# Kernel tuning notes

Hardware: AMD Instinct MI355X
Metric: run time of the kernel (lower is better)

Reference implementation:

```python
import jax, jax.numpy as jnp
import numpy as np

CR = 32  # channels // reduction

def setup_inputs() -> dict:
    key = jax.random.key(0)
    k1, k2 = jax.random.split(key)
    x = jax.random.normal(k1, (1, 64, 8, 32, 32), dtype=jnp.float32)
    W = jax.random.normal(k2, (CR, 64), dtype=jnp.float32) * (1.0 / np.sqrt(64.0))
    bias = jnp.zeros((CR,), dtype=jnp.float32)
    return {"x": x, "W": W, "bias": bias}

def reference(x, W, bias):
    b, c, d, h, w = x.shape
    cr = W.shape[0]
    n = d * h * w
    # 1x1x1 Conv3d == per-voxel linear projection over channels
    x_red = jnp.einsum('oc,bcdhw->bodhw', W, x) + bias[None, :, None, None, None]
    q = x_red.reshape(b, cr, n)          # [b, cr, N]
    k = q                                 # shared projection (q == k)
    v = x.reshape(b, c, n)               # [b, c, N]
    # attn[b, i, j] = <q[:, i], k[:, j]>, softmax over j (dim=2)
    attn = jnp.einsum('bci,bcj->bij', q, k) / jnp.sqrt(jnp.float32(cr))
    attn = jax.nn.softmax(attn, axis=2)
    # out[b, c, m] = sum_n v[b, c, n] * attn[b, n, m]  (torch.bmm(v, attn))
    out = jnp.einsum('bcn,bnm->bcm', v, attn)
    out = out.reshape(b, c, d, h, w)
    return out + x
```

## Files before the change

kernel.cpp:

```cpp
#include <hip/hip_runtime.h>

#define N_TOK 8192

typedef _Float16 f16x8 __attribute__((ext_vector_type(8)));
typedef _Float16 f16x4 __attribute__((ext_vector_type(4)));
typedef float    f32x4 __attribute__((ext_vector_type(4)));

__device__ __forceinline__ f32x4 mfma_k32(f16x8 a, f16x8 b, f32x4 c) {
  return __builtin_amdgcn_mfma_f32_16x16x32_f16(a, b, c, 0, 0, 0);
}
__device__ __forceinline__ f32x4 mfma_k16(f16x4 a, f16x4 b, f32x4 c) {
  return __builtin_amdgcn_mfma_f32_16x16x16f16(a, b, c, 0, 0, 0);
}

#define QSCALE 0.50500977f

__global__ __launch_bounds__(1024) void prep_kernel(
    const float* __restrict__ x, const float* __restrict__ W,
    const float* __restrict__ bias, _Float16* __restrict__ qe,
    _Float16* __restrict__ vht, float* __restrict__ Ln,
    float* __restrict__ out) {
  __shared__ float Wl[32 * 65];
  __shared__ float xl[64 * 36];
  int t = threadIdx.x, b = blockIdx.x;
  int n0 = b * 32;
  if (b < 8) Ln[b * 1024 + t] = 0.f;
  for (int i = t; i < 2048; i += 1024) Wl[(i >> 6) * 65 + (i & 63)] = W[i];
  if (t < 512) {
    int c = t >> 3, j4 = t & 7;
    f32x4 v = *(const f32x4*)(x + c * N_TOK + n0 + j4 * 4);
    *(f32x4*)&xl[c * 36 + j4 * 4] = v;
    *(f32x4*)(out + c * N_TOK + n0 + j4 * 4) = v;
    f16x4 hv;
#pragma unroll
    for (int j = 0; j < 4; ++j) hv[j] = (_Float16)v[j];
    int q = j4 & 3, h = j4 >> 2;
    *(f16x4*)(vht + b * 2048 + c * 32 + q * 8 + h * 4) = hv;
  }
  __syncthreads();
  int nl = t >> 5, o = t & 31;
  float a0 = bias[o], a1 = 0.f;
#pragma unroll
  for (int c = 0; c < 32; ++c) {
    a0 = fmaf(Wl[o * 65 + c], xl[c * 36 + nl], a0);
    a1 = fmaf(Wl[o * 65 + 32 + c], xl[(32 + c) * 36 + nl], a1);
  }
  qe[(n0 + nl) * 32 + o] = (_Float16)((a0 + a1) * QSCALE);
}

__global__ __launch_bounds__(1024) void pass1_kernel(
    const _Float16* __restrict__ qe, float* __restrict__ Ln) {
  __shared__ float Lp[16][64];
  int t = threadIdx.x, b = blockIdx.x;
  int w = t >> 6, lane = t & 63, quad = lane >> 4, l15 = lane & 15;
  int n0 = (b >> 1) * 64;
  int mbase = (b & 1) * 4096 + w * 256;
  f16x8 af[4];
#pragma unroll
  for (int g = 0; g < 4; ++g)
    af[g] = *(const f16x8*)(qe + (n0 + g * 16 + l15) * 32 + quad * 8);
  f32x4 sums[4];
#pragma unroll
  for (int g = 0; g < 4; ++g) sums[g] = f32x4{0.f, 0.f, 0.f, 0.f};
  for (int mt = 0; mt < 8; ++mt) {
    int m0 = mbase + mt * 32;
    f16x8 bf0 = *(const f16x8*)(qe + (m0 + l15) * 32 + quad * 8);
    f16x8 bf1 = *(const f16x8*)(qe + (m0 + 16 + l15) * 32 + quad * 8);
    f32x4 zero = {0.f, 0.f, 0.f, 0.f};
#pragma unroll
    for (int g = 0; g < 4; ++g) {
      f32x4 s0 = mfma_k32(af[g], bf0, zero);
      f32x4 s1 = mfma_k32(af[g], bf1, zero);
#pragma unroll
      for (int r = 0; r < 4; ++r)
        sums[g][r] +=
            __builtin_amdgcn_exp2f(s0[r]) + __builtin_amdgcn_exp2f(s1[r]);
    }
  }
#pragma unroll
  for (int g = 0; g < 4; ++g)
#pragma unroll
    for (int r = 0; r < 4; ++r)
#pragma unroll
      for (int mask = 1; mask < 16; mask <<= 1)
        sums[g][r] += __shfl_xor(sums[g][r], mask, 64);
  if (l15 == 0) {
#pragma unroll
    for (int g = 0; g < 4; ++g)
      *(f32x4*)&Lp[w][g * 16 + quad * 4] = sums[g];
  }
  __syncthreads();
  if (t < 64) {
    float L = 0.f;
#pragma unroll
    for (int ww = 0; ww < 16; ++ww) L += Lp[ww][t];
    unsafeAtomicAdd(Ln + n0 + t, L);
  }
}

__global__ __launch_bounds__(1024, 4) void pass2_kernel(
    const _Float16* __restrict__ qe, const _Float16* __restrict__ vht,
    const float* __restrict__ Ln, float* __restrict__ out) {
  __shared__ float Bl[4096];
  __shared__ float Ot[4 * 64 * 65];
  int t = threadIdx.x, b = blockIdx.x;
  int w = t >> 6, lane = t & 63, quad = lane >> 4, l15 = lane & 15;
  int m0 = (b >> 1) * 64;
  int half = b & 1;
  int nseg = w >> 1, mhalf = w & 1;
  int nhb = half * 4096, nbl0 = nseg * 512;

  for (int i = t; i < 4096; i += 1024)
    Bl[i] = -__builtin_amdgcn_logf(Ln[nhb + i]);
  __syncthreads();

  f16x8 bm[2];
#pragma unroll
  for (int mt = 0; mt < 2; ++mt)
    bm[mt] =
        *(const f16x8*)(qe + (m0 + mhalf * 32 + mt * 16 + l15) * 32 + quad * 8);

  f32x4 acc[4][2];
#pragma unroll
  for (int ct = 0; ct < 4; ++ct)
#pragma unroll
    for (int mt = 0; mt < 2; ++mt) acc[ct][mt] = f32x4{0.f, 0.f, 0.f, 0.f};

  for (int ch = 0; ch < 16; ++ch) {
    int nbl = nbl0 + ch * 32;
    int nb = nhb + nbl;
    f16x8 an0 = *(const f16x8*)(qe + (nb + l15) * 32 + quad * 8);
    f16x8 an1 = *(const f16x8*)(qe + (nb + 16 + l15) * 32 + quad * 8);
    f32x4 nBq0 = *(const f32x4*)&Bl[nbl + quad * 4];
    f32x4 nBq1 = *(const f32x4*)&Bl[nbl + 16 + quad * 4];
    const _Float16* vb = vht + (nb >> 5) * 2048 + l15 * 32 + quad * 8;
    f16x8 av[4];
#pragma unroll
    for (int ct = 0; ct < 4; ++ct)
      av[ct] = *(const f16x8*)(vb + ct * 512);
#pragma unroll
    for (int mt = 0; mt < 2; ++mt) {
      f32x4 s0 = mfma_k32(an0, bm[mt], nBq0);
      f32x4 s1 = mfma_k32(an1, bm[mt], nBq1);
      f16x4 p0, p1;
#pragma unroll
      for (int r = 0; r < 4; ++r) {
        p0[r] = (_Float16)__builtin_amdgcn_exp2f(s0[r]);
        p1[r] = (_Float16)__builtin_amdgcn_exp2f(s1[r]);
      }
#pragma unroll
      for (int ct = 0; ct < 4; ++ct) {
        f16x4 lo, hi;
#pragma unroll
        for (int j = 0; j < 4; ++j) {
          lo[j] = av[ct][j];
          hi[j] = av[ct][j + 4];
        }
        acc[ct][mt] = mfma_k16(lo, p0, acc[ct][mt]);
        acc[ct][mt] = mfma_k16(hi, p1, acc[ct][mt]);
      }
    }
  }

  __syncthreads();
  if (nseg < 4) {
#pragma unroll
    for (int ct = 0; ct < 4; ++ct)
#pragma unroll
      for (int mt = 0; mt < 2; ++mt)
#pragma unroll
        for (int r = 0; r < 4; ++r)
          Ot[(nseg * 64 + ct * 16 + quad * 4 + r) * 65 + mhalf * 32 +
             mt * 16 + l15] = acc[ct][mt][r];
  }
  __syncthreads();
  if (nseg >= 4) {
#pragma unroll
    for (int ct = 0; ct < 4; ++ct)
#pragma unroll
      for (int mt = 0; mt < 2; ++mt)
#pragma unroll
        for (int r = 0; r < 4; ++r)
          Ot[((nseg - 4) * 64 + ct * 16 + quad * 4 + r) * 65 + mhalf * 32 +
             mt * 16 + l15] += acc[ct][mt][r];
  }
  __syncthreads();
  for (int idx = t; idx < 4096; idx += 1024) {
    int cc = idx >> 6, m = idx & 63;
    float v = 0.f;
#pragma unroll
    for (int s = 0; s < 4; ++s) v += Ot[(s * 64 + cc) * 65 + m];
    unsafeAtomicAdd(out + cc * N_TOK + m0 + m, v);
  }
}

extern "C" void kernel_launch(void* const* d_in, const int* in_sizes, int n_in,
                              void* d_out, int out_size, void* d_ws,
                              size_t ws_size, hipStream_t stream) {
  const float* x = (const float*)d_in[0];
  const float* W = (const float*)d_in[1];
  const float* bias = (const float*)d_in[2];
  float* out = (float*)d_out;

  char* ws = (char*)d_ws;
  _Float16* qe = (_Float16*)ws;
  _Float16* vht = (_Float16*)(ws + 524288);
  float* Ln = (float*)(ws + 1572864);

  prep_kernel<<<256, 1024, 0, stream>>>(x, W, bias, qe, vht, Ln, out);
  pass1_kernel<<<256, 1024, 0, stream>>>(qe, Ln);
  pass2_kernel<<<256, 1024, 0, stream>>>(qe, vht, Ln, out);
}
```

Measured before the change: 99.61 us.

## Widen pass2 warp tiles to all 64 query columns and pack exp conversions

Each wave in pass2 now covers all 64 m-columns, with half as many n-chunks per wave, instead of 32 columns over a longer n-range. The change reuses each loaded K/V fragment across twice as many MFMAs, halving global loads of qe/vht per unit of work. It also converts exp results to f16 in pairs with cvt_pkrtz and pre-splits the V fragments. The cost is doubled accumulator registers and a four-stage LDS reduction with more barriers, which may lower occupancy under the 4-block launch bound.

```diff
diff --git a/kernel.cpp b/kernel.cpp
--- a/kernel.cpp
+++ b/kernel.cpp
@@ -4,6 +4,7 @@
 
 typedef _Float16 f16x8 __attribute__((ext_vector_type(8)));
 typedef _Float16 f16x4 __attribute__((ext_vector_type(4)));
+typedef __fp16   fp16x2 __attribute__((ext_vector_type(2)));
 typedef float    f32x4 __attribute__((ext_vector_type(4)));
 
 __device__ __forceinline__ f32x4 mfma_k32(f16x8 a, f16x8 b, f32x4 c) {
@@ -107,26 +108,25 @@
   int w = t >> 6, lane = t & 63, quad = lane >> 4, l15 = lane & 15;
   int m0 = (b >> 1) * 64;
   int half = b & 1;
-  int nseg = w >> 1, mhalf = w & 1;
-  int nhb = half * 4096, nbl0 = nseg * 512;
+  int nhb = half * 4096;
 
   for (int i = t; i < 4096; i += 1024)
     Bl[i] = -__builtin_amdgcn_logf(Ln[nhb + i]);
   __syncthreads();
 
-  f16x8 bm[2];
-#pragma unroll
-  for (int mt = 0; mt < 2; ++mt)
-    bm[mt] =
-        *(const f16x8*)(qe + (m0 + mhalf * 32 + mt * 16 + l15) * 32 + quad * 8);
-
-  f32x4 acc[4][2];
+  f16x8 bm[4];
+#pragma unroll
+  for (int mt = 0; mt < 4; ++mt)
+    bm[mt] = *(const f16x8*)(qe + (m0 + mt * 16 + l15) * 32 + quad * 8);
+
+  f32x4 acc[4][4];
 #pragma unroll
   for (int ct = 0; ct < 4; ++ct)
 #pragma unroll
-    for (int mt = 0; mt < 2; ++mt) acc[ct][mt] = f32x4{0.f, 0.f, 0.f, 0.f};
-
-  for (int ch = 0; ch < 16; ++ch) {
+    for (int mt = 0; mt < 4; ++mt) acc[ct][mt] = f32x4{0.f, 0.f, 0.f, 0.f};
+
+  int nbl0 = w * 256;
+  for (int ch = 0; ch < 8; ++ch) {
     int nbl = nbl0 + ch * 32;
     int nb = nhb + nbl;
     f16x8 an0 = *(const f16x8*)(qe + (nb + l15) * 32 + quad * 8);
@@ -134,55 +134,84 @@
     f32x4 nBq0 = *(const f32x4*)&Bl[nbl + quad * 4];
     f32x4 nBq1 = *(const f32x4*)&Bl[nbl + 16 + quad * 4];
     const _Float16* vb = vht + (nb >> 5) * 2048 + l15 * 32 + quad * 8;
-    f16x8 av[4];
-#pragma unroll
-    for (int ct = 0; ct < 4; ++ct)
-      av[ct] = *(const f16x8*)(vb + ct * 512);
-#pragma unroll
-    for (int mt = 0; mt < 2; ++mt) {
+    f16x4 avlo[4], avhi[4];
+#pragma unroll
+    for (int ct = 0; ct < 4; ++ct) {
+      f16x8 a8 = *(const f16x8*)(vb + ct * 512);
+#pragma unroll
+      for (int j = 0; j < 4; ++j) {
+        avlo[ct][j] = a8[j];
+        avhi[ct][j] = a8[j + 4];
+      }
+    }
+#pragma unroll
+    for (int mt = 0; mt < 4; ++mt) {
       f32x4 s0 = mfma_k32(an0, bm[mt], nBq0);
       f32x4 s1 = mfma_k32(an1, bm[mt], nBq1);
-      f16x4 p0, p1;
-#pragma unroll
-      for (int r = 0; r < 4; ++r) {
-        p0[r] = (_Float16)__builtin_amdgcn_exp2f(s0[r]);
-        p1[r] = (_Float16)__builtin_amdgcn_exp2f(s1[r]);
-      }
+      union {
+        f16x4 v;
+        fp16x2 h[2];
+      } p0, p1;
+      p0.h[0] = __builtin_amdgcn_cvt_pkrtz(__builtin_amdgcn_exp2f(s0[0]),
+                                           __builtin_amdgcn_exp2f(s0[1]));
+      p0.h[1] = __builtin_amdgcn_cvt_pkrtz(__builtin_amdgcn_exp2f(s0[2]),
+                                           __builtin_amdgcn_exp2f(s0[3]));
+      p1.h[0] = __builtin_amdgcn_cvt_pkrtz(__builtin_amdgcn_exp2f(s1[0]),
+                                           __builtin_amdgcn_exp2f(s1[1]));
+      p1.h[1] = __builtin_amdgcn_cvt_pkrtz(__builtin_amdgcn_exp2f(s1[2]),
+                                           __builtin_amdgcn_exp2f(s1[3]));
 #pragma unroll
       for (int ct = 0; ct < 4; ++ct) {
-        f16x4 lo, hi;
-#pragma unroll
-        for (int j = 0; j < 4; ++j) {
-          lo[j] = av[ct][j];
-          hi[j] = av[ct][j + 4];
-        }
-        acc[ct][mt] = mfma_k16(lo, p0, acc[ct][mt]);
-        acc[ct][mt] = mfma_k16(hi, p1, acc[ct][mt]);
+        acc[ct][mt] = mfma_k16(avlo[ct], p0.v, acc[ct][mt]);
+        acc[ct][mt] = mfma_k16(avhi[ct], p1.v, acc[ct][mt]);
       }
     }
   }
 
-  __syncthreads();
-  if (nseg < 4) {
-#pragma unroll
-    for (int ct = 0; ct < 4; ++ct)
-#pragma unroll
-      for (int mt = 0; mt < 2; ++mt)
-#pragma unroll
-        for (int r = 0; r < 4; ++r)
-          Ot[(nseg * 64 + ct * 16 + quad * 4 + r) * 65 + mhalf * 32 +
-             mt * 16 + l15] = acc[ct][mt][r];
-  }
-  __syncthreads();
-  if (nseg >= 4) {
-#pragma unroll
-    for (int ct = 0; ct < 4; ++ct)
-#pragma unroll
-      for (int mt = 0; mt < 2; ++mt)
-#pragma unroll
-        for (int r = 0; r < 4; ++r)
-          Ot[((nseg - 4) * 64 + ct * 16 + quad * 4 + r) * 65 + mhalf * 32 +
-             mt * 16 + l15] += acc[ct][mt][r];
+  int g = w >> 2, set = w & 3;
+  __syncthreads();
+  if (g == 0) {
+#pragma unroll
+    for (int ct = 0; ct < 4; ++ct)
+#pragma unroll
+      for (int mt = 0; mt < 4; ++mt)
+#pragma unroll
+        for (int r = 0; r < 4; ++r)
+          Ot[(set * 64 + ct * 16 + quad * 4 + r) * 65 + mt * 16 + l15] =
+              acc[ct][mt][r];
+  }
+  __syncthreads();
+  if (g == 1) {
+#pragma unroll
+    for (int ct = 0; ct < 4; ++ct)
+#pragma unroll
+      for (int mt = 0; mt < 4; ++mt)
+#pragma unroll
+        for (int r = 0; r < 4; ++r)
+          Ot[(set * 64 + ct * 16 + quad * 4 + r) * 65 + mt * 16 + l15] +=
+              acc[ct][mt][r];
+  }
+  __syncthreads();
+  if (g == 2) {
+#pragma unroll
+    for (int ct = 0; ct < 4; ++ct)
+#pragma unroll
+      for (int mt = 0; mt < 4; ++mt)
+#pragma unroll
+        for (int r = 0; r < 4; ++r)
+          Ot[(set * 64 + ct * 16 + quad * 4 + r) * 65 + mt * 16 + l15] +=
+              acc[ct][mt][r];
+  }
+  __syncthreads();
+  if (g == 3) {
+#pragma unroll
+    for (int ct = 0; ct < 4; ++ct)
+#pragma unroll
+      for (int mt = 0; mt < 4; ++mt)
+#pragma unroll
+        for (int r = 0; r < 4; ++r)
+          Ot[(set * 64 + ct * 16 + quad * 4 + r) * 65 + mt * 16 + l15] +=
+              acc[ct][mt][r];
   }
   __syncthreads();
   for (int idx = t; idx < 4096; idx += 1024) {
```

Result: slower. 122.6 us (+23.1%).
